# Kernel optimization log

Hardware: AMD Instinct MI355X
Metric: run time of the kernel (lower is better)

The kernel has to match this reference:

```python
import jax, jax.numpy as jnp
import numpy as np

B, S, D, H = 2, 2048, 1024, 16
DH = D // H


def setup_inputs() -> dict:
    key = jax.random.key(0)
    ks = jax.random.split(key, 5)
    scale = 0.02
    return {
        "X": jax.random.normal(ks[0], (B, S, D), jnp.float32),
        "Wq": jax.random.normal(ks[1], (H, D, DH), jnp.float32) * scale,
        "Wk": jax.random.normal(ks[2], (H, D, DH), jnp.float32) * scale,
        "Wv": jax.random.normal(ks[3], (H, D, DH), jnp.float32) * scale,
        "Wo": jax.random.normal(ks[4], (D, D), jnp.float32) * scale,
        "bo": jnp.zeros((D,), jnp.float32),
    }


def reference(X, Wq, Wk, Wv, Wo, bo):
    # Per-head projections, batched over heads: [B,H,S,DH]
    Q = jnp.einsum('bsd,hde->bhse', X, Wq)
    K = jnp.einsum('bsd,hde->bhse', X, Wk)
    V = jnp.einsum('bsd,hde->bhse', X, Wv)
    # Scores scaled by sqrt(d_model) exactly as in the source (not sqrt(d_head))
    A = jnp.einsum('bhse,bhte->bhst', Q, K) / jnp.sqrt(jnp.float32(D))
    A = jax.nn.softmax(A, axis=-1)  # no mask in the source
    O = jnp.einsum('bhst,bhte->bhse', A, V)  # [B,H,S,DH]
    # Concat heads -> [B,S,D], then output projection
    O = jnp.transpose(O, (0, 2, 1, 3)).reshape(B, S, D)
    return O @ Wo + bo
```

## Files before the change

### kernel.cpp

```cpp
#include <hip/hip_runtime.h>
#include <math.h>

static constexpr int Bc  = 2;
static constexpr int Sc  = 2048;
static constexpr int Dc  = 1024;
static constexpr int Hc  = 16;
static constexpr int DHc = 64;

typedef short bf16x8 __attribute__((ext_vector_type(8)));
typedef float f32x4  __attribute__((ext_vector_type(4)));

static constexpr float LOG2E = 1.4426950408889634f;

static __device__ __forceinline__ unsigned short f2bf(float x) {
  union { float f; unsigned u; } v; v.f = x;
  unsigned r = v.u + 0x7FFFu + ((v.u >> 16) & 1u);
  return (unsigned short)(r >> 16);
}
static __device__ __forceinline__ float bf2f(unsigned short u) {
  union { unsigned u; float f; } v; v.u = ((unsigned)u) << 16;
  return v.f;
}
static __device__ __forceinline__ unsigned pk2bf_trunc(float a, float b) {
  return __builtin_amdgcn_perm(__float_as_uint(b), __float_as_uint(a), 0x07060302u);
}
#if __has_builtin(__builtin_amdgcn_exp2f)
#define EXP2F(x) __builtin_amdgcn_exp2f(x)
#else
#define EXP2F(x) exp2f(x)
#endif

static __device__ __forceinline__ void gload16(const void* g, void* l) {
  __builtin_amdgcn_global_load_lds(
      (const __attribute__((address_space(1))) void*)g,
      (__attribute__((address_space(3))) void*)l, 16, 0, 0);
}

__global__ __launch_bounds__(256) void prep(
    const float* __restrict__ Wq, const float* __restrict__ Wk,
    const float* __restrict__ Wv, const float* __restrict__ Wo,
    const float* __restrict__ X,
    unsigned short* __restrict__ Wt3, unsigned short* __restrict__ Wot,
    unsigned short* __restrict__ Xb) {
  const int z = blockIdx.z;
  if (z == 4) {
    size_t base = ((size_t)blockIdx.y * 16 + blockIdx.x) * 4096;
#pragma unroll
    for (int it = 0; it < 16; ++it) {
      size_t i = base + it * 256 + threadIdx.x;
      float4 v = ((const float4*)X)[i];
      ushort4 u; u.x = f2bf(v.x); u.y = f2bf(v.y); u.z = f2bf(v.z); u.w = f2bf(v.w);
      ((ushort4*)Xb)[i] = u;
    }
    return;
  }
  __shared__ unsigned short T[64][68];
  const float* src; unsigned short* dst;
  int srcld, dstld, r0, c0;
  if (z < 3) {
    const float* W = (z == 0) ? Wq : (z == 1) ? Wk : Wv;
    unsigned short* Wt = Wt3 + (size_t)z * Dc * Dc;
    int h = blockIdx.y;
    src = W + (size_t)h * Dc * DHc;  srcld = DHc; r0 = blockIdx.x * 64; c0 = 0;
    dst = Wt + (size_t)h * DHc * Dc; dstld = Dc;
  } else {
    src = Wo;  srcld = Dc; r0 = blockIdx.x * 64; c0 = blockIdx.y * 64;
    dst = Wot; dstld = Dc;
  }
#pragma unroll
  for (int it = 0; it < 16; ++it) {
    int idx = it * 256 + threadIdx.x;
    int r = idx >> 6, c = idx & 63;
    T[c][r] = f2bf(src[(size_t)(r0 + r) * srcld + c0 + c]);
  }
  __syncthreads();
#pragma unroll
  for (int it = 0; it < 4; ++it) {
    int idx = it * 256 + threadIdx.x;
    int c = idx >> 4, r4 = (idx & 15) * 4;
    ushort4 u = *(const ushort4*)&T[c][r4];
    *(ushort4*)&dst[(size_t)(c0 + c) * dstld + r0 + r4] = u;
  }
}

__global__ __launch_bounds__(256) void qkv_gemm(
    const unsigned short* __restrict__ Xb, const unsigned short* __restrict__ Wt3,
    unsigned short* __restrict__ Qb, unsigned short* __restrict__ Kb,
    unsigned short* __restrict__ Vtb) {
  __shared__ alignas(16) unsigned char smem[35072];
  unsigned short (*As)[64] = (unsigned short(*)[64])smem;
  unsigned short (*Bs)[64] = (unsigned short(*)[64])(smem + 16384);

  const int tid = threadIdx.x;
  const int wv = tid >> 6, lane = tid & 63;
  const int ln = tid & 15, qd = (tid >> 4) & 3;
  const int wm = wv >> 1, wn = wv & 1;
  const int m0 = blockIdx.x * 128;
  const int y  = blockIdx.y;
  const int n0 = y * 128;
  const int which = y >> 3;
  const int lr = lane >> 3;
  const int lcs = ((lane & 7) ^ lr) * 8;

  f32x4 acc[4][4];
#pragma unroll
  for (int mt = 0; mt < 4; ++mt)
#pragma unroll
    for (int nt = 0; nt < 4; ++nt) acc[mt][nt] = (f32x4){0.f, 0.f, 0.f, 0.f};

  for (int k0 = 0; k0 < Dc; k0 += 64) {
    __syncthreads();
#pragma unroll
    for (int t = 0; t < 4; ++t) {
      gload16(Xb  + (size_t)(m0 + wv * 32 + t * 8 + lr) * Dc + k0 + lcs, &As[wv * 32 + t * 8][0]);
      gload16(Wt3 + (size_t)(n0 + wv * 32 + t * 8 + lr) * Dc + k0 + lcs, &Bs[wv * 32 + t * 8][0]);
    }
    __syncthreads();
#pragma unroll
    for (int ks = 0; ks < 2; ++ks) {
      const int pa = ((ks * 4 + qd) ^ (ln & 7)) * 8;
      bf16x8 af[4], bf[4];
#pragma unroll
      for (int mt = 0; mt < 4; ++mt)
        af[mt] = *(const bf16x8*)&As[wm * 64 + mt * 16 + ln][pa];
#pragma unroll
      for (int nt = 0; nt < 4; ++nt)
        bf[nt] = *(const bf16x8*)&Bs[wn * 64 + nt * 16 + ln][pa];
#pragma unroll
      for (int mt = 0; mt < 4; ++mt)
#pragma unroll
        for (int nt = 0; nt < 4; ++nt)
          acc[mt][nt] = __builtin_amdgcn_mfma_f32_16x16x32_bf16(af[mt], bf[nt], acc[mt][nt], 0, 0, 0);
    }
  }

  const int b = m0 >> 11, s0 = m0 & 2047;

  if (which < 2) {
    unsigned short* Out = (which == 0) ? Qb : Kb;
    const float scale = (which == 0) ? (LOG2E / 32.0f) : 1.0f;
#pragma unroll
    for (int mt = 0; mt < 4; ++mt)
#pragma unroll
      for (int r = 0; r < 4; ++r) {
        int s = s0 + wm * 64 + mt * 16 + qd * 4 + r;
#pragma unroll
        for (int nt = 0; nt < 4; ++nt) {
          int n = (n0 & 1023) + wn * 64 + nt * 16 + ln;
          int h = n >> 6, e = n & 63;
          Out[(((size_t)b * Hc + h) * Sc + s) * DHc + e] = f2bf(acc[mt][nt][r] * scale);
        }
      }
  } else {
    __syncthreads();
    unsigned short* Ts = (unsigned short*)smem;
    const int hb = (y & 7) * 2;
#pragma unroll
    for (int mt = 0; mt < 4; ++mt)
#pragma unroll
      for (int r = 0; r < 4; ++r)
#pragma unroll
        for (int nt = 0; nt < 4; ++nt)
          Ts[(wm * 64 + mt * 16 + qd * 4 + r) * 137 + wn * 64 + nt * 16 + ln] =
              f2bf(acc[mt][nt][r]);
    __syncthreads();
#pragma unroll
    for (int hh = 0; hh < 2; ++hh) {
      int bh = b * Hc + hb + hh;
#pragma unroll
      for (int it = 0; it < 8; ++it) {
        int idx = it * 256 + tid;
        int e = idx >> 5, s4 = (idx & 31) * 4;
        ushort4 u;
        u.x = Ts[(s4 + 0) * 137 + hh * 64 + e];
        u.y = Ts[(s4 + 1) * 137 + hh * 64 + e];
        u.z = Ts[(s4 + 2) * 137 + hh * 64 + e];
        u.w = Ts[(s4 + 3) * 137 + hh * 64 + e];
        *(ushort4*)&Vtb[((size_t)bh * DHc + e) * Sc + s0 + s4] = u;
      }
    }
  }
}

__global__ __launch_bounds__(256) void attn_partial(
    const unsigned short* __restrict__ Qb, const unsigned short* __restrict__ Kb,
    const unsigned short* __restrict__ Vtb,
    unsigned short* __restrict__ Opart, float* __restrict__ lpart) {
  __shared__ alignas(16) unsigned short Ks[64][64];
  __shared__ alignas(16) unsigned short Vts[64][64];
  __shared__ alignas(16) unsigned short Ps[128][64];

  const int tid = threadIdx.x;
  const int wv = tid >> 6, lane = tid & 63;
  const int ln = tid & 15, qd = (tid >> 4) & 3;
  const int sT = blockIdx.x, bh = blockIdx.y, sp = blockIdx.z;
  const int lr = lane >> 3;
  const int lcs = ((lane & 7) ^ lr) * 8;

  bf16x8 qf[2][2];
  const size_t qrow0 = (size_t)bh * Sc + sT * 128 + wv * 32;
#pragma unroll
  for (int mt = 0; mt < 2; ++mt)
#pragma unroll
    for (int ks = 0; ks < 2; ++ks)
      qf[mt][ks] = *(const bf16x8*)&Qb[(qrow0 + mt * 16 + ln) * DHc + ks * 32 + qd * 8];

  bf16x8 vones;
#pragma unroll
  for (int j = 0; j < 8; ++j) vones[j] = (short)0x3F80;

  f32x4 o[2][4], lacc[2];
#pragma unroll
  for (int mt = 0; mt < 2; ++mt) {
    lacc[mt] = (f32x4){0.f, 0.f, 0.f, 0.f};
#pragma unroll
    for (int et = 0; et < 4; ++et) o[mt][et] = (f32x4){0.f, 0.f, 0.f, 0.f};
  }

  for (int kb = sp * 16; kb < sp * 16 + 16; ++kb) {
    __syncthreads();
#pragma unroll
    for (int t = 0; t < 2; ++t) {
      gload16(Kb  + ((size_t)bh * Sc + kb * 64 + wv * 16 + t * 8 + lr) * DHc + lcs,
              &Ks[wv * 16 + t * 8][0]);
      gload16(Vtb + ((size_t)bh * DHc + wv * 16 + t * 8 + lr) * Sc + kb * 64 + lcs,
              &Vts[wv * 16 + t * 8][0]);
    }
    __syncthreads();

    f32x4 st[2][4];
#pragma unroll
    for (int mt = 0; mt < 2; ++mt)
#pragma unroll
      for (int nt = 0; nt < 4; ++nt) st[mt][nt] = (f32x4){0.f, 0.f, 0.f, 0.f};
#pragma unroll
    for (int ks = 0; ks < 2; ++ks) {
      const int pa = ((ks * 4 + qd) ^ (ln & 7)) * 8;
#pragma unroll
      for (int nt = 0; nt < 4; ++nt) {
        bf16x8 kf = *(const bf16x8*)&Ks[nt * 16 + ln][pa];
#pragma unroll
        for (int mt = 0; mt < 2; ++mt)
          st[mt][nt] = __builtin_amdgcn_mfma_f32_16x16x32_bf16(kf, qf[mt][ks], st[mt][nt], 0, 0, 0);
      }
    }

#pragma unroll
    for (int mt = 0; mt < 2; ++mt) {
      const int prow = wv * 32 + mt * 16 + ln;
#pragma unroll
      for (int nt = 0; nt < 4; ++nt) {
        float p0 = EXP2F(st[mt][nt][0]);
        float p1 = EXP2F(st[mt][nt][1]);
        float p2 = EXP2F(st[mt][nt][2]);
        float p3 = EXP2F(st[mt][nt][3]);
        uint2 w;
        w.x = pk2bf_trunc(p0, p1);
        w.y = pk2bf_trunc(p2, p3);
        int ppos = ((2 * nt + (qd >> 1)) ^ (ln & 7)) * 8 + (qd & 1) * 4;
        *(uint2*)&Ps[prow][ppos] = w;
      }
    }
    __syncthreads();

#pragma unroll
    for (int ks = 0; ks < 2; ++ks) {
      const int pa = ((ks * 4 + qd) ^ (ln & 7)) * 8;
      bf16x8 pf[2];
#pragma unroll
      for (int mt = 0; mt < 2; ++mt) {
        pf[mt] = *(const bf16x8*)&Ps[wv * 32 + mt * 16 + ln][pa];
        lacc[mt] = __builtin_amdgcn_mfma_f32_16x16x32_bf16(pf[mt], vones, lacc[mt], 0, 0, 0);
      }
#pragma unroll
      for (int et = 0; et < 4; ++et) {
        bf16x8 vf = *(const bf16x8*)&Vts[et * 16 + ln][pa];
#pragma unroll
        for (int mt = 0; mt < 2; ++mt)
          o[mt][et] = __builtin_amdgcn_mfma_f32_16x16x32_bf16(pf[mt], vf, o[mt][et], 0, 0, 0);
      }
    }
  }

  const size_t pbase = ((size_t)sp * 512 + bh * 16 + sT) * 128;
  if (ln == 0) {
#pragma unroll
    for (int mt = 0; mt < 2; ++mt)
#pragma unroll
      for (int r = 0; r < 4; ++r)
        lpart[pbase + wv * 32 + mt * 16 + qd * 4 + r] = lacc[mt][r];
  }
#pragma unroll
  for (int mt = 0; mt < 2; ++mt)
#pragma unroll
    for (int r = 0; r < 4; ++r) {
      int row = wv * 32 + mt * 16 + qd * 4 + r;
#pragma unroll
      for (int et = 0; et < 4; ++et)
        Opart[(pbase + row) * DHc + et * 16 + ln] = f2bf(o[mt][et][r]);
    }
}

__global__ __launch_bounds__(256) void combine(
    const unsigned short* __restrict__ Opart, const float* __restrict__ lpart,
    unsigned short* __restrict__ Ocat) {
  const int sT = blockIdx.x, bh = blockIdx.y, tid = threadIdx.x;
  const int b = bh >> 4, h = bh & 15;
  const size_t p0 = ((size_t)bh * 16 + sT) * 128;
  const size_t p1 = ((size_t)512 + bh * 16 + sT) * 128;
#pragma unroll
  for (int it = 0; it < 8; ++it) {
    int idx = it * 256 + tid;
    int row = idx >> 4, c4 = (idx & 15) * 4;
    ushort4 u0 = *(const ushort4*)&Opart[(p0 + row) * DHc + c4];
    ushort4 u1 = *(const ushort4*)&Opart[(p1 + row) * DHc + c4];
    float inv = 1.0f / (lpart[p0 + row] + lpart[p1 + row]);
    ushort4 w;
    w.x = f2bf((bf2f(u0.x) + bf2f(u1.x)) * inv);
    w.y = f2bf((bf2f(u0.y) + bf2f(u1.y)) * inv);
    w.z = f2bf((bf2f(u0.z) + bf2f(u1.z)) * inv);
    w.w = f2bf((bf2f(u0.w) + bf2f(u1.w)) * inv);
    *(ushort4*)&Ocat[((size_t)b * Sc + sT * 128 + row) * Dc + h * DHc + c4] = w;
  }
}

__global__ __launch_bounds__(256) void out_gemm(
    const unsigned short* __restrict__ Ab, const unsigned short* __restrict__ Wot,
    const float* __restrict__ bo, float* __restrict__ Out) {
  __shared__ alignas(16) unsigned short As[64][64];
  __shared__ alignas(16) unsigned short Bs[128][64];

  const int tid = threadIdx.x;
  const int wv = tid >> 6, lane = tid & 63;
  const int ln = tid & 15, qd = (tid >> 4) & 3;
  const int wm = wv >> 1, wn = wv & 1;
  const int m0 = blockIdx.x * 64, n0 = blockIdx.y * 128;
  const int lr = lane >> 3;
  const int lcs = ((lane & 7) ^ lr) * 8;

  f32x4 acc[2][4];
#pragma unroll
  for (int mt = 0; mt < 2; ++mt)
#pragma unroll
    for (int nt = 0; nt < 4; ++nt) acc[mt][nt] = (f32x4){0.f, 0.f, 0.f, 0.f};

  for (int k0 = 0; k0 < Dc; k0 += 64) {
    __syncthreads();
#pragma unroll
    for (int t = 0; t < 2; ++t)
      gload16(Ab + (size_t)(m0 + wv * 16 + t * 8 + lr) * Dc + k0 + lcs, &As[wv * 16 + t * 8][0]);
#pragma unroll
    for (int t = 0; t < 4; ++t)
      gload16(Wot + (size_t)(n0 + wv * 32 + t * 8 + lr) * Dc + k0 + lcs, &Bs[wv * 32 + t * 8][0]);
    __syncthreads();
#pragma unroll
    for (int ks = 0; ks < 2; ++ks) {
      const int pa = ((ks * 4 + qd) ^ (ln & 7)) * 8;
      bf16x8 af[2], bf[4];
#pragma unroll
      for (int mt = 0; mt < 2; ++mt)
        af[mt] = *(const bf16x8*)&As[wm * 32 + mt * 16 + ln][pa];
#pragma unroll
      for (int nt = 0; nt < 4; ++nt)
        bf[nt] = *(const bf16x8*)&Bs[wn * 64 + nt * 16 + ln][pa];
#pragma unroll
      for (int mt = 0; mt < 2; ++mt)
#pragma unroll
        for (int nt = 0; nt < 4; ++nt)
          acc[mt][nt] = __builtin_amdgcn_mfma_f32_16x16x32_bf16(af[mt], bf[nt], acc[mt][nt], 0, 0, 0);
    }
  }

  float bias[4];
#pragma unroll
  for (int nt = 0; nt < 4; ++nt) bias[nt] = bo[n0 + wn * 64 + nt * 16 + ln];

#pragma unroll
  for (int mt = 0; mt < 2; ++mt)
#pragma unroll
    for (int r = 0; r < 4; ++r) {
      int m = m0 + wm * 32 + mt * 16 + qd * 4 + r;
#pragma unroll
      for (int nt = 0; nt < 4; ++nt)
        Out[(size_t)m * Dc + n0 + wn * 64 + nt * 16 + ln] = acc[mt][nt][r] + bias[nt];
    }
}

extern "C" void kernel_launch(void* const* d_in, const int* in_sizes, int n_in,
                              void* d_out, int out_size, void* d_ws, size_t ws_size,
                              hipStream_t stream) {
  (void)in_sizes; (void)n_in; (void)out_size; (void)ws_size;
  const float* X  = (const float*)d_in[0];
  const float* Wq = (const float*)d_in[1];
  const float* Wk = (const float*)d_in[2];
  const float* Wv = (const float*)d_in[3];
  const float* Wo = (const float*)d_in[4];
  const float* bo = (const float*)d_in[5];
  float* out = (float*)d_out;

  const size_t nX = (size_t)Bc * Sc * Dc;
  unsigned short* Xb    = (unsigned short*)d_ws;
  unsigned short* Wt3   = Xb + nX;
  unsigned short* Wot   = Wt3 + (size_t)3 * Dc * Dc;
  unsigned short* Qb    = Wot + (size_t)Dc * Dc;
  unsigned short* Kb    = Qb + nX;
  unsigned short* Vtb   = Kb + nX;
  unsigned short* Opart = Vtb + nX;
  float* lpart = (float*)(Opart + 2 * nX);
  unsigned short* Ocat = Xb;

  prep<<<dim3(16, 16, 5), 256, 0, stream>>>(Wq, Wk, Wv, Wo, X, Wt3, Wot, Xb);
  qkv_gemm<<<dim3(32, 24), 256, 0, stream>>>(Xb, Wt3, Qb, Kb, Vtb);
  attn_partial<<<dim3(16, 32, 2), 256, 0, stream>>>(Qb, Kb, Vtb, Opart, lpart);
  combine<<<dim3(16, 32), 256, 0, stream>>>(Opart, lpart, Ocat);
  out_gemm<<<dim3(64, 8), 256, 0, stream>>>(Ocat, Wot, bo, out);
}
```

Before: 199.4 us.

## Halve attention query tile to 64 rows and stage Q/K epilogue through LDS

The attention kernel now processes 64 query rows per block (16 per wave) instead of 128, doubling the grid to 2048 blocks and halving per-wave registers and LDS for P, with combine adjusted to match. Separately, the Q/K projection epilogue writes results into shared memory and then emits 16-byte coalesced row stores instead of scattered 2-byte stores. The smaller attention tile raises occupancy and block count but halves reuse of each K/V tile loaded into LDS, increasing K/V global traffic.

```diff
diff --git a/kernel.cpp b/kernel.cpp
--- a/kernel.cpp
+++ b/kernel.cpp
@@ -135,24 +135,32 @@
   }
 
   const int b = m0 >> 11, s0 = m0 & 2047;
+  __syncthreads();
 
   if (which < 2) {
     unsigned short* Out = (which == 0) ? Qb : Kb;
     const float scale = (which == 0) ? (LOG2E / 32.0f) : 1.0f;
+    unsigned short* Ts = (unsigned short*)smem;
 #pragma unroll
     for (int mt = 0; mt < 4; ++mt)
 #pragma unroll
-      for (int r = 0; r < 4; ++r) {
-        int s = s0 + wm * 64 + mt * 16 + qd * 4 + r;
-#pragma unroll
-        for (int nt = 0; nt < 4; ++nt) {
-          int n = (n0 & 1023) + wn * 64 + nt * 16 + ln;
-          int h = n >> 6, e = n & 63;
-          Out[(((size_t)b * Hc + h) * Sc + s) * DHc + e] = f2bf(acc[mt][nt][r] * scale);
-        }
-      }
+      for (int r = 0; r < 4; ++r)
+#pragma unroll
+        for (int nt = 0; nt < 4; ++nt)
+          Ts[(wm * 64 + mt * 16 + qd * 4 + r) * 136 + wn * 64 + nt * 16 + ln] =
+              f2bf(acc[mt][nt][r] * scale);
+    __syncthreads();
+    const int row = tid >> 1;
+    const int half = tid & 1;
+    const int nbase = (n0 & 1023) + half * 64;
+    const int h = nbase >> 6;
+    unsigned short* gp = Out + (((size_t)b * Hc + h) * Sc + s0 + row) * DHc;
+#pragma unroll
+    for (int it = 0; it < 8; ++it) {
+      ulonglong2 u = *(const ulonglong2*)&Ts[row * 136 + half * 64 + it * 8];
+      *(ulonglong2*)&gp[it * 8] = u;
+    }
   } else {
-    __syncthreads();
     unsigned short* Ts = (unsigned short*)smem;
     const int hb = (y & 7) * 2;
 #pragma unroll
@@ -188,7 +196,7 @@
     unsigned short* __restrict__ Opart, float* __restrict__ lpart) {
   __shared__ alignas(16) unsigned short Ks[64][64];
   __shared__ alignas(16) unsigned short Vts[64][64];
-  __shared__ alignas(16) unsigned short Ps[128][64];
+  __shared__ alignas(16) unsigned short Ps[64][64];
 
   const int tid = threadIdx.x;
   const int wv = tid >> 6, lane = tid & 63;
@@ -197,25 +205,20 @@
   const int lr = lane >> 3;
   const int lcs = ((lane & 7) ^ lr) * 8;
 
-  bf16x8 qf[2][2];
-  const size_t qrow0 = (size_t)bh * Sc + sT * 128 + wv * 32;
-#pragma unroll
-  for (int mt = 0; mt < 2; ++mt)
-#pragma unroll
-    for (int ks = 0; ks < 2; ++ks)
-      qf[mt][ks] = *(const bf16x8*)&Qb[(qrow0 + mt * 16 + ln) * DHc + ks * 32 + qd * 8];
+  bf16x8 qf[2];
+  const size_t qrow0 = (size_t)bh * Sc + sT * 64 + wv * 16;
+#pragma unroll
+  for (int ks = 0; ks < 2; ++ks)
+    qf[ks] = *(const bf16x8*)&Qb[(qrow0 + ln) * DHc + ks * 32 + qd * 8];
 
   bf16x8 vones;
 #pragma unroll
   for (int j = 0; j < 8; ++j) vones[j] = (short)0x3F80;
 
-  f32x4 o[2][4], lacc[2];
-#pragma unroll
-  for (int mt = 0; mt < 2; ++mt) {
-    lacc[mt] = (f32x4){0.f, 0.f, 0.f, 0.f};
-#pragma unroll
-    for (int et = 0; et < 4; ++et) o[mt][et] = (f32x4){0.f, 0.f, 0.f, 0.f};
-  }
+  f32x4 o[4], lacc;
+  lacc = (f32x4){0.f, 0.f, 0.f, 0.f};
+#pragma unroll
+  for (int et = 0; et < 4; ++et) o[et] = (f32x4){0.f, 0.f, 0.f, 0.f};
 
   for (int kb = sp * 16; kb < sp * 16 + 16; ++kb) {
     __syncthreads();
@@ -228,77 +231,60 @@
     }
     __syncthreads();
 
-    f32x4 st[2][4];
-#pragma unroll
-    for (int mt = 0; mt < 2; ++mt)
-#pragma unroll
-      for (int nt = 0; nt < 4; ++nt) st[mt][nt] = (f32x4){0.f, 0.f, 0.f, 0.f};
+    f32x4 st[4];
+#pragma unroll
+    for (int nt = 0; nt < 4; ++nt) st[nt] = (f32x4){0.f, 0.f, 0.f, 0.f};
 #pragma unroll
     for (int ks = 0; ks < 2; ++ks) {
       const int pa = ((ks * 4 + qd) ^ (ln & 7)) * 8;
 #pragma unroll
       for (int nt = 0; nt < 4; ++nt) {
         bf16x8 kf = *(const bf16x8*)&Ks[nt * 16 + ln][pa];
-#pragma unroll
-        for (int mt = 0; mt < 2; ++mt)
-          st[mt][nt] = __builtin_amdgcn_mfma_f32_16x16x32_bf16(kf, qf[mt][ks], st[mt][nt], 0, 0, 0);
+        st[nt] = __builtin_amdgcn_mfma_f32_16x16x32_bf16(kf, qf[ks], st[nt], 0, 0, 0);
       }
     }
 
-#pragma unroll
-    for (int mt = 0; mt < 2; ++mt) {
-      const int prow = wv * 32 + mt * 16 + ln;
-#pragma unroll
-      for (int nt = 0; nt < 4; ++nt) {
-        float p0 = EXP2F(st[mt][nt][0]);
-        float p1 = EXP2F(st[mt][nt][1]);
-        float p2 = EXP2F(st[mt][nt][2]);
-        float p3 = EXP2F(st[mt][nt][3]);
-        uint2 w;
-        w.x = pk2bf_trunc(p0, p1);
-        w.y = pk2bf_trunc(p2, p3);
-        int ppos = ((2 * nt + (qd >> 1)) ^ (ln & 7)) * 8 + (qd & 1) * 4;
-        *(uint2*)&Ps[prow][ppos] = w;
-      }
+    const int prow = wv * 16 + ln;
+#pragma unroll
+    for (int nt = 0; nt < 4; ++nt) {
+      float p0 = EXP2F(st[nt][0]);
+      float p1 = EXP2F(st[nt][1]);
+      float p2 = EXP2F(st[nt][2]);
+      float p3 = EXP2F(st[nt][3]);
+      uint2 w;
+      w.x = pk2bf_trunc(p0, p1);
+      w.y = pk2bf_trunc(p2, p3);
+      int ppos = ((2 * nt + (qd >> 1)) ^ (ln & 7)) * 8 + (qd & 1) * 4;
+      *(uint2*)&Ps[prow][ppos] = w;
     }
     __syncthreads();
 
 #pragma unroll
     for (int ks = 0; ks < 2; ++ks) {
       const int pa = ((ks * 4 + qd) ^ (ln & 7)) * 8;
-      bf16x8 pf[2];
-#pragma unroll
-      for (int mt = 0; mt < 2; ++mt) {
-        pf[mt] = *(const bf16x8*)&Ps[wv * 32 + mt * 16 + ln][pa];
-        lacc[mt] = __builtin_amdgcn_mfma_f32_16x16x32_bf16(pf[mt], vones, lacc[mt], 0, 0, 0);
-      }
+      bf16x8 pf = *(const bf16x8*)&Ps[wv * 16 + ln][pa];
+      lacc = __builtin_amdgcn_mfma_f32_16x16x32_bf16(pf, vones, lacc, 0, 0, 0);
 #pragma unroll
       for (int et = 0; et < 4; ++et) {
         bf16x8 vf = *(const bf16x8*)&Vts[et * 16 + ln][pa];
-#pragma unroll
-        for (int mt = 0; mt < 2; ++mt)
-          o[mt][et] = __builtin_amdgcn_mfma_f32_16x16x32_bf16(pf[mt], vf, o[mt][et], 0, 0, 0);
+        o[et] = __builtin_amdgcn_mfma_f32_16x16x32_bf16(pf, vf, o[et], 0, 0, 0);
       }
     }
   }
 
-  const size_t pbase = ((size_t)sp * 512 + bh * 16 + sT) * 128;
+  const size_t pbase = ((size_t)sp * 1024 + bh * 32 + sT) * 64;
   if (ln == 0) {
 #pragma unroll
-    for (int mt = 0; mt < 2; ++mt)
-#pragma unroll
-      for (int r = 0; r < 4; ++r)
-        lpart[pbase + wv * 32 + mt * 16 + qd * 4 + r] = lacc[mt][r];
-  }
-#pragma unroll
-  for (int mt = 0; mt < 2; ++mt)
-#pragma unroll
-    for (int r = 0; r < 4; ++r) {
-      int row = wv * 32 + mt * 16 + qd * 4 + r;
-#pragma unroll
-      for (int et = 0; et < 4; ++et)
-        Opart[(pbase + row) * DHc + et * 16 + ln] = f2bf(o[mt][et][r]);
-    }
+    for (int r = 0; r < 4; ++r)
+      lpart[pbase + wv * 16 + qd * 4 + r] = lacc[r];
+  }
+#pragma unroll
+  for (int r = 0; r < 4; ++r) {
+    int row = wv * 16 + qd * 4 + r;
+#pragma unroll
+    for (int et = 0; et < 4; ++et)
+      Opart[(pbase + row) * DHc + et * 16 + ln] = f2bf(o[et][r]);
+  }
 }
 
 __global__ __launch_bounds__(256) void combine(
@@ -306,10 +292,10 @@
     unsigned short* __restrict__ Ocat) {
   const int sT = blockIdx.x, bh = blockIdx.y, tid = threadIdx.x;
   const int b = bh >> 4, h = bh & 15;
-  const size_t p0 = ((size_t)bh * 16 + sT) * 128;
-  const size_t p1 = ((size_t)512 + bh * 16 + sT) * 128;
-#pragma unroll
-  for (int it = 0; it < 8; ++it) {
+  const size_t p0 = ((size_t)bh * 32 + sT) * 64;
+  const size_t p1 = ((size_t)1024 + bh * 32 + sT) * 64;
+#pragma unroll
+  for (int it = 0; it < 4; ++it) {
     int idx = it * 256 + tid;
     int row = idx >> 4, c4 = (idx & 15) * 4;
     ushort4 u0 = *(const ushort4*)&Opart[(p0 + row) * DHc + c4];
@@ -320,7 +306,7 @@
     w.y = f2bf((bf2f(u0.y) + bf2f(u1.y)) * inv);
     w.z = f2bf((bf2f(u0.z) + bf2f(u1.z)) * inv);
     w.w = f2bf((bf2f(u0.w) + bf2f(u1.w)) * inv);
-    *(ushort4*)&Ocat[((size_t)b * Sc + sT * 128 + row) * Dc + h * DHc + c4] = w;
+    *(ushort4*)&Ocat[((size_t)b * Sc + sT * 64 + row) * Dc + h * DHc + c4] = w;
   }
 }
 
@@ -411,7 +397,7 @@
 
   prep<<<dim3(16, 16, 5), 256, 0, stream>>>(Wq, Wk, Wv, Wo, X, Wt3, Wot, Xb);
   qkv_gemm<<<dim3(32, 24), 256, 0, stream>>>(Xb, Wt3, Qb, Kb, Vtb);
-  attn_partial<<<dim3(16, 32, 2), 256, 0, stream>>>(Qb, Kb, Vtb, Opart, lpart);
-  combine<<<dim3(16, 32), 256, 0, stream>>>(Opart, lpart, Ocat);
+  attn_partial<<<dim3(32, 32, 2), 256, 0, stream>>>(Qb, Kb, Vtb, Opart, lpart);
+  combine<<<dim3(32, 32), 256, 0, stream>>>(Opart, lpart, Ocat);
   out_gemm<<<dim3(64, 8), 256, 0, stream>>>(Ocat, Wot, bo, out);
 }
```

Result: slower. 204.0 us (+2.3%).
